# Optimization experiments

Measured on AMD Instinct MI355X. Metric: run time of the kernel, lower is better.

## Reference

```python
import jax, jax.numpy as jnp
import numpy as np

NUM_LAYER = 5
NUM_FEATURES = 128
DIM = 256
NUM_BOND_TYPE = 6
NUM_BOND_DIR = 3
BN_EPS = 1e-5


def setup_inputs() -> dict:
    key = jax.random.key(0)
    ks = jax.random.split(key, 16)
    N, E = 100000, 400000
    x = jax.random.normal(ks[0], (N, NUM_FEATURES), dtype=jnp.float32)
    edge_index = jax.random.randint(ks[1], (2, E), 0, N, dtype=jnp.int32)
    edge_attr = jax.random.randint(ks[2], (E, 2), 0, 3, dtype=jnp.int32)
    s = 0.05
    Wl = jax.random.normal(ks[3], (NUM_FEATURES, DIM), dtype=jnp.float32) * s
    bl = jnp.zeros((DIM,), dtype=jnp.float32)
    W1 = jax.random.normal(ks[4], (NUM_LAYER, DIM, 2 * DIM), dtype=jnp.float32) * s
    b1 = jnp.zeros((NUM_LAYER, 2 * DIM), dtype=jnp.float32)
    W2 = jax.random.normal(ks[5], (NUM_LAYER, 2 * DIM, DIM), dtype=jnp.float32) * s
    b2 = jnp.zeros((NUM_LAYER, DIM), dtype=jnp.float32)
    E1 = jax.random.normal(ks[6], (NUM_LAYER, NUM_BOND_TYPE, DIM), dtype=jnp.float32) * s
    E2 = jax.random.normal(ks[7], (NUM_LAYER, NUM_BOND_DIR, DIM), dtype=jnp.float32) * s
    gamma = jnp.ones((NUM_LAYER, DIM), dtype=jnp.float32)
    beta = jnp.zeros((NUM_LAYER, DIM), dtype=jnp.float32)
    return {"x": x, "edge_index": edge_index, "edge_attr": edge_attr,
            "Wl": Wl, "bl": bl, "W1": W1, "b1": b1, "W2": W2, "b2": b2,
            "E1": E1, "E2": E2, "gamma": gamma, "beta": beta}


def reference(x, edge_index, edge_attr, Wl, bl, W1, b1, W2, b2, E1, E2, gamma, beta):
    N = x.shape[0]
    src, dst = edge_index[0], edge_index[1]
    bt, bd = edge_attr[:, 0], edge_attr[:, 1]
    # input projection + activation
    h = jax.nn.relu(x @ Wl + bl)  # [N, D]
    for l in range(NUM_LAYER):
        # edge embeddings (real edges) + self-loop embedding (attr = [4, 0])
        eemb = E1[l][bt] + E2[l][bd]                      # [E, D]
        self_emb = E1[l][4] + E2[l][0]                    # [D]
        msg = h[src] + eemb                               # gather + add
        agg = jax.ops.segment_sum(msg, dst, num_segments=N)
        agg = agg + h + self_emb                          # self-loop messages
        # 2-layer MLP update
        hid = jax.nn.relu(agg @ W1[l] + b1[l])
        out = hid @ W2[l] + b2[l]
        # BatchNorm1d (training mode: batch stats, biased variance)
        mean = jnp.mean(out, axis=0)
        var = jnp.mean((out - mean) ** 2, axis=0)
        h = gamma[l] * (out - mean) * jax.lax.rsqrt(var + BN_EPS) + beta[l]
    # JK = 'last'
    return h
```

## Files before the change

### kernel.cpp

```cpp
#include <hip/hip_runtime.h>
#include <hip/hip_bf16.h>


typedef __bf16 bf16x8 __attribute__((ext_vector_type(8)));
typedef __bf16 bf16x4 __attribute__((ext_vector_type(4)));
typedef float f32x4 __attribute__((ext_vector_type(4)));

#define LDSTRIDE 40

__global__ __launch_bounds__(256, 2)
void gemm0_kernel(const float* __restrict__ Av, const __bf16* __restrict__ BT,
                  const float* __restrict__ bias, float* __restrict__ Cv,
                  int M, int K, int Nc)
{
    __shared__ __bf16 As[128 * LDSTRIDE];
    __shared__ __bf16 Bs[128 * LDSTRIDE];

    const int tid  = threadIdx.x;
    const int wave = tid >> 6;
    const int lane = tid & 63;
    const int quad = lane >> 4;
    const int l16  = lane & 15;
    const int wm   = wave >> 1;
    const int wn   = wave & 1;

    const int col0 = blockIdx.x * 128;
    const int row0 = blockIdx.y * 128;

    f32x4 acc[4][4];
#pragma unroll
    for (int mt = 0; mt < 4; ++mt)
#pragma unroll
        for (int nt = 0; nt < 4; ++nt) acc[mt][nt] = (f32x4){0.f, 0.f, 0.f, 0.f};

    const int srow = tid >> 1;
    const int scol = (tid & 1) * 16;
    const int a_row = row0 + srow;
    const bool a_ok = (a_row < M);
    const __bf16* Bp = BT + (size_t)(col0 + srow) * K + scol;

    for (int k0 = 0; k0 < K; k0 += 32) {
        bf16x8 a0, a1;
        const float* Ap = Av + (size_t)a_row * K + k0 + scol;
        f32x4 x0 = {0,0,0,0}, x1 = {0,0,0,0}, x2 = {0,0,0,0}, x3 = {0,0,0,0};
        if (a_ok) {
            x0 = *(const f32x4*)(Ap);
            x1 = *(const f32x4*)(Ap + 4);
            x2 = *(const f32x4*)(Ap + 8);
            x3 = *(const f32x4*)(Ap + 12);
        }
#pragma unroll
        for (int j = 0; j < 4; ++j) {
            a0[j] = (__bf16)x0[j]; a0[4 + j] = (__bf16)x1[j];
            a1[j] = (__bf16)x2[j]; a1[4 + j] = (__bf16)x3[j];
        }
        bf16x8 b0 = *(const bf16x8*)(Bp + k0);
        bf16x8 b1 = *(const bf16x8*)(Bp + k0 + 8);

        __syncthreads();
        *(bf16x8*)&As[srow * LDSTRIDE + scol]     = a0;
        *(bf16x8*)&As[srow * LDSTRIDE + scol + 8] = a1;
        *(bf16x8*)&Bs[srow * LDSTRIDE + scol]     = b0;
        *(bf16x8*)&Bs[srow * LDSTRIDE + scol + 8] = b1;
        __syncthreads();

        bf16x8 af[4], bfr[4];
#pragma unroll
        for (int mt = 0; mt < 4; ++mt)
            af[mt] = *(const bf16x8*)&As[(wm * 64 + mt * 16 + l16) * LDSTRIDE + quad * 8];
#pragma unroll
        for (int nt = 0; nt < 4; ++nt)
            bfr[nt] = *(const bf16x8*)&Bs[(wn * 64 + nt * 16 + l16) * LDSTRIDE + quad * 8];

#pragma unroll
        for (int mt = 0; mt < 4; ++mt)
#pragma unroll
            for (int nt = 0; nt < 4; ++nt)
                acc[mt][nt] = __builtin_amdgcn_mfma_f32_16x16x32_bf16(
                    af[mt], bfr[nt], acc[mt][nt], 0, 0, 0);
    }

#pragma unroll
    for (int nt = 0; nt < 4; ++nt) {
        const int col = col0 + wn * 64 + nt * 16 + l16;
        const float b = bias[col];
#pragma unroll
        for (int mt = 0; mt < 4; ++mt) {
#pragma unroll
            for (int r = 0; r < 4; ++r) {
                const int row = row0 + wm * 64 + mt * 16 + quad * 4 + r;
                if (row < M) {
                    float v = fmaxf(acc[mt][nt][r] + b, 0.f);
                    Cv[(size_t)row * Nc + col] = v;
                }
            }
        }
    }
}


__global__ __launch_bounds__(256, 4)
void fused_mlp_kernel(const __bf16* __restrict__ aggb,
                      const __bf16* __restrict__ W1T, const float* __restrict__ b1,
                      const __bf16* __restrict__ W2T, const float* __restrict__ b2,
                      float* __restrict__ out, float* __restrict__ sums, int M)
{
    __shared__ __bf16 As[64 * 256];
    __shared__ __bf16 hidS[64 * 64];

    const int tid  = threadIdx.x;
    const int wave = tid >> 6;
    const int lane = tid & 63;
    const int quad = lane >> 4;
    const int l16  = lane & 15;
    const int row0 = blockIdx.x * 64;

    {
        const int srow = tid >> 2;
        const int gb8  = (tid & 3) * 8;
        const int m = row0 + srow;
        bf16x8 v[8];
        if (m < M) {
            const __bf16* Ap = aggb + (size_t)m * 256 + gb8 * 8;
#pragma unroll
            for (int j = 0; j < 8; ++j) v[j] = *(const bf16x8*)(Ap + j * 8);
        } else {
#pragma unroll
            for (int j = 0; j < 8; ++j)
#pragma unroll
                for (int q = 0; q < 8; ++q) v[j][q] = (__bf16)0.f;
        }
#pragma unroll
        for (int j = 0; j < 8; ++j) {
            const int sg = (gb8 + j) ^ (srow & 7);
            *(bf16x8*)&As[srow * 256 + sg * 8] = v[j];
        }
    }
    __syncthreads();

    const int cb = wave * 64;
    f32x4 acc2[4][4];
#pragma unroll
    for (int mt = 0; mt < 4; ++mt)
#pragma unroll
        for (int nt = 0; nt < 4; ++nt) acc2[mt][nt] = (f32x4){0.f, 0.f, 0.f, 0.f};

    const __bf16* W1p = W1T + (size_t)(wave * 16 + l16) * 256 + quad * 8;
    const __bf16* W2p = W2T + (size_t)(cb + l16) * 512 + quad * 8;

#pragma unroll 1
    for (int c = 0; c <= 8; ++c) {
        if (c >= 1) {
#pragma unroll
            for (int kkl = 0; kkl < 2; ++kkl) {
                bf16x8 W2f[4], Hf[4];
#pragma unroll
                for (int nt = 0; nt < 4; ++nt)
                    W2f[nt] = *(const bf16x8*)(W2p + (size_t)(nt * 16) * 512
                                               + (c - 1) * 64 + kkl * 32);
#pragma unroll
                for (int mt = 0; mt < 4; ++mt) {
                    const int row = mt * 16 + l16;
                    const int sg = (kkl * 4 + quad) ^ (row & 7);
                    Hf[mt] = *(const bf16x8*)&hidS[row * 64 + sg * 8];
                }
#pragma unroll
                for (int mt = 0; mt < 4; ++mt)
#pragma unroll
                    for (int nt = 0; nt < 4; ++nt)
                        acc2[mt][nt] = __builtin_amdgcn_mfma_f32_16x16x32_bf16(
                            Hf[mt], W2f[nt], acc2[mt][nt], 0, 0, 0);
            }
        }

        if (c < 8) {
            __syncthreads();

            f32x4 acc1[4];
#pragma unroll
            for (int mt = 0; mt < 4; ++mt) acc1[mt] = (f32x4){0.f, 0.f, 0.f, 0.f};
            const __bf16* p = W1p + (size_t)(c * 64) * 256;
#pragma unroll
            for (int kk = 0; kk < 8; ++kk) {
                bf16x8 W1f = *(const bf16x8*)(p + kk * 32);
                const int sg = (kk * 4 + quad) ^ (l16 & 7);
                bf16x8 af[4];
#pragma unroll
                for (int mt = 0; mt < 4; ++mt)
                    af[mt] = *(const bf16x8*)&As[(mt * 16 + l16) * 256 + sg * 8];
#pragma unroll
                for (int mt = 0; mt < 4; ++mt)
                    acc1[mt] = __builtin_amdgcn_mfma_f32_16x16x32_bf16(
                        af[mt], W1f, acc1[mt], 0, 0, 0);
            }

            {
                const int lcol = wave * 16 + l16;
                const float bb = b1[c * 64 + lcol];
                const int colgrp = lcol >> 3;
                const int c7 = lcol & 7;
#pragma unroll
                for (int mt = 0; mt < 4; ++mt)
#pragma unroll
                    for (int r = 0; r < 4; ++r) {
                        const int row = mt * 16 + quad * 4 + r;
                        float v = fmaxf(acc1[mt][r] + bb, 0.f);
                        hidS[row * 64 + ((colgrp ^ (row & 7)) << 3) + c7] = (__bf16)v;
                    }
            }
            __syncthreads();
        }
    }

    float* srep = sums + (blockIdx.x & 7) * 512;
#pragma unroll
    for (int nt = 0; nt < 4; ++nt) {
        const int col = cb + nt * 16 + l16;
        const float bb = b2[col];
        float s = 0.f, ss = 0.f;
#pragma unroll
        for (int mt = 0; mt < 4; ++mt) {
#pragma unroll
            for (int r = 0; r < 4; ++r) {
                const int row = row0 + mt * 16 + quad * 4 + r;
                if (row < M) {
                    float v = acc2[mt][nt][r] + bb;
                    out[(size_t)row * 256 + col] = v;
                    s += v; ss += v * v;
                }
            }
        }
        s += __shfl_xor(s, 16); ss += __shfl_xor(ss, 16);
        s += __shfl_xor(s, 32); ss += __shfl_xor(ss, 32);
        if (lane < 16) {
            atomicAdd(&srep[col], s);
            atomicAdd(&srep[256 + col], ss);
        }
    }
}

__global__ void convert_wt_kernel(const float* __restrict__ W, __bf16* __restrict__ WT,
                                  int K, int Nc, int total)
{
    int i = blockIdx.x * 256 + threadIdx.x;
    if (i >= total) return;
    int kn = K * Nc;
    int l = i / kn;
    int rem = i - l * kn;
    int n = rem / K;
    int k = rem - n * K;
    WT[i] = (__bf16)W[(size_t)l * kn + (size_t)k * Nc + n];
}


__global__ void zero_counts_kernel(int* __restrict__ counts, int N)
{
    int i = blockIdx.x * 256 + threadIdx.x;
    if (i < N) counts[i] = 0;
}

__global__ void hist_kernel(const int* __restrict__ ei, int* __restrict__ counts, int E)
{
    int e = blockIdx.x * 256 + threadIdx.x;
    if (e < E) atomicAdd(&counts[ei[E + e]], 1);
}

__global__ void scan1_kernel(const int* __restrict__ counts, int* __restrict__ partial,
                             int* __restrict__ blocksums, int N)
{
    __shared__ int sm[256];
    int i = blockIdx.x * 256 + threadIdx.x;
    int v = (i < N) ? counts[i] : 0;
    sm[threadIdx.x] = v;
    __syncthreads();
    for (int off = 1; off < 256; off <<= 1) {
        int t = 0;
        if ((int)threadIdx.x >= off) t = sm[threadIdx.x - off];
        __syncthreads();
        if ((int)threadIdx.x >= off) sm[threadIdx.x] += t;
        __syncthreads();
    }
    if (i < N) partial[i] = sm[threadIdx.x] - v;
    if (threadIdx.x == 255) blocksums[blockIdx.x] = sm[255];
}

__global__ void scan2_kernel(int* __restrict__ blocksums, int NB)
{
    __shared__ int sm[1024];
    int v = ((int)threadIdx.x < NB) ? blocksums[threadIdx.x] : 0;
    sm[threadIdx.x] = v;
    __syncthreads();
    for (int off = 1; off < 1024; off <<= 1) {
        int t = 0;
        if ((int)threadIdx.x >= off) t = sm[threadIdx.x - off];
        __syncthreads();
        if ((int)threadIdx.x >= off) sm[threadIdx.x] += t;
        __syncthreads();
    }
    if ((int)threadIdx.x < NB) blocksums[threadIdx.x] = sm[threadIdx.x] - v;
}

__global__ void scan3_kernel(const int* __restrict__ partial, const int* __restrict__ blocksums,
                             int* __restrict__ rowptr, int* __restrict__ woff, int N, int E)
{
    int i = blockIdx.x * 256 + threadIdx.x;
    if (i < N) {
        int v = partial[i] + blocksums[blockIdx.x];
        rowptr[i] = v;
        woff[i] = v;
    }
    if (i == 0) rowptr[N] = E;
}

__global__ void scatter_sort_kernel(const int* __restrict__ ei, const int* __restrict__ ea,
                                    int* __restrict__ woff, int* __restrict__ sorted, int E)
{
    int e = blockIdx.x * 256 + threadIdx.x;
    if (e >= E) return;
    int dst = ei[E + e];
    int src = ei[e];
    int c = ea[2 * e] * 3 + ea[2 * e + 1];
    int pos = atomicAdd(&woff[dst], 1);
    sorted[pos] = (src << 4) | c;
}


__global__ void build_table_kernel(const float* __restrict__ E1, const float* __restrict__ E2,
                                   int l, float* __restrict__ tab, float* __restrict__ selfemb,
                                   float* __restrict__ sums)
{
    int b = blockIdx.x;
    int t = threadIdx.x;
    const float* e1 = E1 + (size_t)l * 6 * 256;
    const float* e2 = E2 + (size_t)l * 3 * 256;
    if (b < 9) {
        tab[b * 256 + t] = e1[(b / 3) * 256 + t] + e2[(b % 3) * 256 + t];
    } else {
        selfemb[t] = e1[4 * 256 + t] + e2[0 * 256 + t];
#pragma unroll
        for (int r = 0; r < 16; ++r) sums[r * 256 + t] = 0.f;
    }
}

template<int APPLY_BN>
__global__ __launch_bounds__(256)
void gather_kernel(const float* __restrict__ out, const int* __restrict__ rowptr,
                   const int* __restrict__ sorted, const float* __restrict__ tab,
                   const float* __restrict__ selfemb, const float* __restrict__ scsh,
                   __bf16* __restrict__ aggb, int N)
{
    int n = blockIdx.x * 4 + (threadIdx.x >> 6);
    if (n >= N) return;
    int lane = threadIdx.x & 63;
    int f = lane * 4;

    f32x4 sc, sh;
    if (APPLY_BN) {
        sc = *(const f32x4*)(scsh + f);
        sh = *(const f32x4*)(scsh + 256 + f);
    }

    int r0 = rowptr[n];
    int r1 = rowptr[n + 1];

    f32x4 hv = *(const f32x4*)(out + (size_t)n * 256 + f);
    if (APPLY_BN) hv = hv * sc + sh;
    f32x4 acc = hv + *(const f32x4*)(selfemb + f);

    int e = r0;
#pragma unroll 1
    for (; e + 4 <= r1; e += 4) {
        int v0 = sorted[e + 0];
        int v1 = sorted[e + 1];
        int v2 = sorted[e + 2];
        int v3 = sorted[e + 3];
        f32x4 x0 = *(const f32x4*)(out + (size_t)(v0 >> 4) * 256 + f);
        f32x4 x1 = *(const f32x4*)(out + (size_t)(v1 >> 4) * 256 + f);
        f32x4 x2 = *(const f32x4*)(out + (size_t)(v2 >> 4) * 256 + f);
        f32x4 x3 = *(const f32x4*)(out + (size_t)(v3 >> 4) * 256 + f);
        f32x4 t0 = *(const f32x4*)(tab + (v0 & 15) * 256 + f);
        f32x4 t1 = *(const f32x4*)(tab + (v1 & 15) * 256 + f);
        f32x4 t2 = *(const f32x4*)(tab + (v2 & 15) * 256 + f);
        f32x4 t3 = *(const f32x4*)(tab + (v3 & 15) * 256 + f);
        if (APPLY_BN) {
            x0 = x0 * sc + sh; x1 = x1 * sc + sh;
            x2 = x2 * sc + sh; x3 = x3 * sc + sh;
        }
        acc += (x0 + t0) + (x1 + t1);
        acc += (x2 + t2) + (x3 + t3);
    }
#pragma unroll 1
    for (; e < r1; ++e) {
        int v = sorted[e];
        f32x4 xv = *(const f32x4*)(out + (size_t)(v >> 4) * 256 + f);
        if (APPLY_BN) xv = xv * sc + sh;
        acc += xv + *(const f32x4*)(tab + (v & 15) * 256 + f);
    }
    bf16x4 o;
#pragma unroll
    for (int j = 0; j < 4; ++j) o[j] = (__bf16)acc[j];
    *(bf16x4*)(aggb + (size_t)n * 256 + f) = o;
}

__global__ void bn_finalize_kernel(const float* __restrict__ sums,
                                   const float* __restrict__ gamma,
                                   const float* __restrict__ beta,
                                   int l, int M, float* __restrict__ scsh)
{
    int c = threadIdx.x;
    float s = 0.f, ss = 0.f;
#pragma unroll
    for (int r = 0; r < 8; ++r) {
        s  += sums[r * 512 + c];
        ss += sums[r * 512 + 256 + c];
    }
    float inv = 1.f / (float)M;
    float mean = s * inv;
    float var = ss * inv - mean * mean;
    float sc = gamma[l * 256 + c] * rsqrtf(var + 1e-5f);
    scsh[c] = sc;
    scsh[256 + c] = beta[l * 256 + c] - mean * sc;
}

__global__ __launch_bounds__(256)
void bn_apply_kernel(const float* __restrict__ out, const float* __restrict__ scsh,
                     float* __restrict__ h, int total4)
{
    int i = blockIdx.x * 256 + threadIdx.x;
    if (i >= total4) return;
    int cg = i & 63;
    f32x4 sc = ((const f32x4*)scsh)[cg];
    f32x4 sh = ((const f32x4*)scsh)[64 + cg];
    f32x4 v = ((const f32x4*)out)[i];
    ((f32x4*)h)[i] = v * sc + sh;
}

extern "C" void kernel_launch(void* const* d_in, const int* in_sizes, int n_in,
                              void* d_out, int out_size, void* d_ws, size_t ws_size,
                              hipStream_t stream)
{
    const float* x     = (const float*)d_in[0];
    const int*   ei    = (const int*)d_in[1];
    const int*   ea    = (const int*)d_in[2];
    const float* Wl    = (const float*)d_in[3];
    const float* bl    = (const float*)d_in[4];
    const float* W1    = (const float*)d_in[5];
    const float* b1    = (const float*)d_in[6];
    const float* W2    = (const float*)d_in[7];
    const float* b2    = (const float*)d_in[8];
    const float* E1    = (const float*)d_in[9];
    const float* E2    = (const float*)d_in[10];
    const float* gamma = (const float*)d_in[11];
    const float* beta  = (const float*)d_in[12];

    const int N = in_sizes[0] / 128;
    const int E = in_sizes[1] / 2;

    __bf16* aggb = (__bf16*)d_out;
    float*  hfin = (float*)d_out;

    float*  out  = (float*)d_ws;
    __bf16* WlT  = (__bf16*)(out + (size_t)N * 256);
    __bf16* W1T  = WlT + 256 * 128;
    __bf16* W2T  = W1T + 5 * 512 * 256;
    float*  tab  = (float*)(W2T + 5 * 256 * 512);
    float*  selfemb = tab + 9 * 256;
    float*  sums = selfemb + 256;
    float*  scsh = sums + 4096;
    int*    counts = (int*)(scsh + 512);
    int*    partial = counts + N;
    int*    rowptr  = partial + N;
    int*    woff    = rowptr + N + 1;
    int*    sorted  = woff + N;
    int*    blocksums = sorted + E;

    const int NB = (N + 255) / 256;
    const int EB = (E + 255) / 256;

    zero_counts_kernel<<<NB, 256, 0, stream>>>(counts, N);
    hist_kernel<<<EB, 256, 0, stream>>>(ei, counts, E);
    scan1_kernel<<<NB, 256, 0, stream>>>(counts, partial, blocksums, N);
    scan2_kernel<<<1, 1024, 0, stream>>>(blocksums, NB);
    scan3_kernel<<<NB, 256, 0, stream>>>(partial, blocksums, rowptr, woff, N, E);
    scatter_sort_kernel<<<EB, 256, 0, stream>>>(ei, ea, woff, sorted, E);

    convert_wt_kernel<<<(128 * 256 + 255) / 256, 256, 0, stream>>>(Wl, WlT, 128, 256, 128 * 256);
    convert_wt_kernel<<<(5 * 256 * 512 + 255) / 256, 256, 0, stream>>>(W1, W1T, 256, 512, 5 * 256 * 512);
    convert_wt_kernel<<<(5 * 512 * 256 + 255) / 256, 256, 0, stream>>>(W2, W2T, 512, 256, 5 * 512 * 256);

    const int mtiles128 = (N + 127) / 128;
    const int mtiles64  = (N + 63) / 64;
    const int total4 = N * 64;
    const int ew_blocks = (total4 + 255) / 256;
    const int gb = (N + 3) / 4;

    gemm0_kernel<<<dim3(2, mtiles128), 256, 0, stream>>>(x, WlT, bl, out, N, 128, 256);

    for (int l = 0; l < 5; ++l) {
        build_table_kernel<<<10, 256, 0, stream>>>(E1, E2, l, tab, selfemb, sums);
        if (l == 0)
            gather_kernel<0><<<gb, 256, 0, stream>>>(out, rowptr, sorted, tab, selfemb,
                                                     scsh, aggb, N);
        else
            gather_kernel<1><<<gb, 256, 0, stream>>>(out, rowptr, sorted, tab, selfemb,
                                                     scsh, aggb, N);
        fused_mlp_kernel<<<mtiles64, 256, 0, stream>>>(
            aggb, W1T + (size_t)l * 512 * 256, b1 + l * 512,
            W2T + (size_t)l * 256 * 512, b2 + l * 256, out, sums, N);
        bn_finalize_kernel<<<1, 256, 0, stream>>>(sums, gamma, beta, l, N, scsh);
    }
    bn_apply_kernel<<<ew_blocks, 256, 0, stream>>>(out, scsh, hfin, total4);
}
```

Before: 1.436 ms.

## Enlarge fused MLP tile to 128 rows with 8 waves and prefetch W1

New measurement: 1.359 ms. 5.3% less time.

```diff
diff --git a/kernel.cpp b/kernel.cpp
--- a/kernel.cpp
+++ b/kernel.cpp
@@ -99,21 +99,21 @@
 }
 
 
-__global__ __launch_bounds__(256, 4)
+__global__ __launch_bounds__(512, 2)
 void fused_mlp_kernel(const __bf16* __restrict__ aggb,
                       const __bf16* __restrict__ W1T, const float* __restrict__ b1,
                       const __bf16* __restrict__ W2T, const float* __restrict__ b2,
                       float* __restrict__ out, float* __restrict__ sums, int M)
 {
-    __shared__ __bf16 As[64 * 256];
-    __shared__ __bf16 hidS[64 * 64];
+    __shared__ __bf16 As[128 * 256];
+    __shared__ __bf16 hidS[128 * 128];
 
     const int tid  = threadIdx.x;
-    const int wave = tid >> 6;
+    const int wid  = tid >> 6;
     const int lane = tid & 63;
     const int quad = lane >> 4;
     const int l16  = lane & 15;
-    const int row0 = blockIdx.x * 64;
+    const int row0 = blockIdx.x * 128;
 
     {
         const int srow = tid >> 2;
@@ -136,90 +136,97 @@
             *(bf16x8*)&As[srow * 256 + sg * 8] = v[j];
         }
     }
+
+    f32x4 acc2[8][2];
+#pragma unroll
+    for (int mt = 0; mt < 8; ++mt)
+#pragma unroll
+        for (int nt = 0; nt < 2; ++nt) acc2[mt][nt] = (f32x4){0.f, 0.f, 0.f, 0.f};
+
+    const __bf16* W1p = W1T + (size_t)(wid * 16 + l16) * 256 + quad * 8;
+    const __bf16* W2p = W2T + (size_t)(wid * 32 + l16) * 512 + quad * 8;
+
+    bf16x8 w1f[2][8];
+#pragma unroll
+    for (int kk = 0; kk < 8; ++kk)
+        w1f[0][kk] = *(const bf16x8*)(W1p + (size_t)0 + kk * 32);
+
     __syncthreads();
 
-    const int cb = wave * 64;
-    f32x4 acc2[4][4];
-#pragma unroll
-    for (int mt = 0; mt < 4; ++mt)
-#pragma unroll
-        for (int nt = 0; nt < 4; ++nt) acc2[mt][nt] = (f32x4){0.f, 0.f, 0.f, 0.f};
-
-    const __bf16* W1p = W1T + (size_t)(wave * 16 + l16) * 256 + quad * 8;
-    const __bf16* W2p = W2T + (size_t)(cb + l16) * 512 + quad * 8;
-
-#pragma unroll 1
-    for (int c = 0; c <= 8; ++c) {
-        if (c >= 1) {
-#pragma unroll
-            for (int kkl = 0; kkl < 2; ++kkl) {
-                bf16x8 W2f[4], Hf[4];
-#pragma unroll
-                for (int nt = 0; nt < 4; ++nt)
-                    W2f[nt] = *(const bf16x8*)(W2p + (size_t)(nt * 16) * 512
-                                               + (c - 1) * 64 + kkl * 32);
-#pragma unroll
-                for (int mt = 0; mt < 4; ++mt) {
-                    const int row = mt * 16 + l16;
-                    const int sg = (kkl * 4 + quad) ^ (row & 7);
-                    Hf[mt] = *(const bf16x8*)&hidS[row * 64 + sg * 8];
+#pragma unroll
+    for (int c = 0; c < 4; ++c) {
+        const int cur = c & 1;
+        const int nxt = cur ^ 1;
+
+        bf16x8 w2f[4][2];
+#pragma unroll
+        for (int kkl = 0; kkl < 4; ++kkl)
+#pragma unroll
+            for (int nt = 0; nt < 2; ++nt)
+                w2f[kkl][nt] = *(const bf16x8*)(W2p + (size_t)(nt * 16) * 512
+                                                + c * 128 + kkl * 32);
+
+        f32x4 acc1[8];
+#pragma unroll
+        for (int mt = 0; mt < 8; ++mt) acc1[mt] = (f32x4){0.f, 0.f, 0.f, 0.f};
+#pragma unroll
+        for (int kk = 0; kk < 8; ++kk) {
+            const int sg = (kk * 4 + quad) ^ (l16 & 7);
+#pragma unroll
+            for (int mt = 0; mt < 8; ++mt) {
+                bf16x8 af = *(const bf16x8*)&As[(mt * 16 + l16) * 256 + sg * 8];
+                acc1[mt] = __builtin_amdgcn_mfma_f32_16x16x32_bf16(
+                    af, w1f[cur][kk], acc1[mt], 0, 0, 0);
+            }
+        }
+
+        __syncthreads();
+
+        {
+            const int lcol = wid * 16 + l16;
+            const float bb = b1[c * 128 + lcol];
+            const int cg = lcol >> 3;
+            const int c7 = lcol & 7;
+#pragma unroll
+            for (int mt = 0; mt < 8; ++mt)
+#pragma unroll
+                for (int r = 0; r < 4; ++r) {
+                    const int row = mt * 16 + quad * 4 + r;
+                    float v = fmaxf(acc1[mt][r] + bb, 0.f);
+                    hidS[row * 128 + ((cg ^ (row & 7)) << 3) + c7] = (__bf16)v;
                 }
-#pragma unroll
-                for (int mt = 0; mt < 4; ++mt)
-#pragma unroll
-                    for (int nt = 0; nt < 4; ++nt)
-                        acc2[mt][nt] = __builtin_amdgcn_mfma_f32_16x16x32_bf16(
-                            Hf[mt], W2f[nt], acc2[mt][nt], 0, 0, 0);
+        }
+        __syncthreads();
+
+        if (c < 3) {
+#pragma unroll
+            for (int kk = 0; kk < 8; ++kk)
+                w1f[nxt][kk] = *(const bf16x8*)(W1p + (size_t)((c + 1) * 128) * 256
+                                                + kk * 32);
+        }
+
+#pragma unroll
+        for (int kkl = 0; kkl < 4; ++kkl) {
+#pragma unroll
+            for (int mt = 0; mt < 8; ++mt) {
+                const int sg = (kkl * 4 + quad) ^ (l16 & 7);
+                bf16x8 hf = *(const bf16x8*)&hidS[(mt * 16 + l16) * 128 + sg * 8];
+#pragma unroll
+                for (int nt = 0; nt < 2; ++nt)
+                    acc2[mt][nt] = __builtin_amdgcn_mfma_f32_16x16x32_bf16(
+                        hf, w2f[kkl][nt], acc2[mt][nt], 0, 0, 0);
             }
         }
-
-        if (c < 8) {
-            __syncthreads();
-
-            f32x4 acc1[4];
-#pragma unroll
-            for (int mt = 0; mt < 4; ++mt) acc1[mt] = (f32x4){0.f, 0.f, 0.f, 0.f};
-            const __bf16* p = W1p + (size_t)(c * 64) * 256;
-#pragma unroll
-            for (int kk = 0; kk < 8; ++kk) {
-                bf16x8 W1f = *(const bf16x8*)(p + kk * 32);
-                const int sg = (kk * 4 + quad) ^ (l16 & 7);
-                bf16x8 af[4];
-#pragma unroll
-                for (int mt = 0; mt < 4; ++mt)
-                    af[mt] = *(const bf16x8*)&As[(mt * 16 + l16) * 256 + sg * 8];
-#pragma unroll
-                for (int mt = 0; mt < 4; ++mt)
-                    acc1[mt] = __builtin_amdgcn_mfma_f32_16x16x32_bf16(
-                        af[mt], W1f, acc1[mt], 0, 0, 0);
-            }
-
-            {
-                const int lcol = wave * 16 + l16;
-                const float bb = b1[c * 64 + lcol];
-                const int colgrp = lcol >> 3;
-                const int c7 = lcol & 7;
-#pragma unroll
-                for (int mt = 0; mt < 4; ++mt)
-#pragma unroll
-                    for (int r = 0; r < 4; ++r) {
-                        const int row = mt * 16 + quad * 4 + r;
-                        float v = fmaxf(acc1[mt][r] + bb, 0.f);
-                        hidS[row * 64 + ((colgrp ^ (row & 7)) << 3) + c7] = (__bf16)v;
-                    }
-            }
-            __syncthreads();
-        }
     }
 
     float* srep = sums + (blockIdx.x & 7) * 512;
 #pragma unroll
-    for (int nt = 0; nt < 4; ++nt) {
-        const int col = cb + nt * 16 + l16;
+    for (int nt = 0; nt < 2; ++nt) {
+        const int col = wid * 32 + nt * 16 + l16;
         const float bb = b2[col];
         float s = 0.f, ss = 0.f;
 #pragma unroll
-        for (int mt = 0; mt < 4; ++mt) {
+        for (int mt = 0; mt < 8; ++mt) {
 #pragma unroll
             for (int r = 0; r < 4; ++r) {
                 const int row = row0 + mt * 16 + quad * 4 + r;
@@ -489,7 +496,6 @@
     convert_wt_kernel<<<(5 * 512 * 256 + 255) / 256, 256, 0, stream>>>(W2, W2T, 512, 256, 5 * 512 * 256);
 
     const int mtiles128 = (N + 127) / 128;
-    const int mtiles64  = (N + 63) / 64;
     const int total4 = N * 64;
     const int ew_blocks = (total4 + 255) / 256;
     const int gb = (N + 3) / 4;
@@ -504,7 +510,7 @@
         else
             gather_kernel<1><<<gb, 256, 0, stream>>>(out, rowptr, sorted, tab, selfemb,
                                                      scsh, aggb, N);
-        fused_mlp_kernel<<<mtiles64, 256, 0, stream>>>(
+        fused_mlp_kernel<<<mtiles128, 512, 0, stream>>>(
             aggb, W1T + (size_t)l * 512 * 256, b1 + l * 512,
             W2T + (size_t)l * 256 * 512, b2 + l * 256, out, sums, N);
         bn_finalize_kernel<<<1, 256, 0, stream>>>(sums, gamma, beta, l, N, scsh);
```
